# Performance work log

Measured on AMD Instinct MI355X. Metric: run time of the kernel, lower is better.

Reference implementation:

```python
import jax, jax.numpy as jnp
import numpy as np

EPS = 1e-5

def _ln(x, g, b):
    m = jnp.mean(x, axis=-1, keepdims=True)
    v = jnp.var(x, axis=-1, keepdims=True)
    return (x - m) / jnp.sqrt(v + EPS) * g + b

def _partition(x, nw):
    b, h, w, c = x.shape
    x = x.reshape(b, nw, h // nw, nw, w // nw, c).transpose(0, 1, 3, 2, 4, 5)
    return x.reshape(b * nw * nw, h // nw, w // nw, c)

def _merge(x, nw):
    b_, h, w, c = x.shape
    b = b_ // (nw * nw)
    x = x.reshape(b, nw, nw, h, w, c).transpose(0, 1, 3, 2, 4, 5)
    return x.reshape(b, nw * h, nw * w, c)

def _window_attn(q, k, v, width, height, nw, mask):
    b, _, c = q.shape
    q = q.reshape(b, height, width, c)
    k = k.reshape(b, height, width, c)
    v = v.reshape(b, height, width, c)
    sh, sw = (height // nw) // 2, (width // nw) // 2
    q = jnp.roll(q, (-sh, -sw), (1, 2))
    k = jnp.roll(k, (-sh, -sw), (1, 2))
    v = jnp.roll(v, (-sh, -sw), (1, 2))
    q = _partition(q, nw); k = _partition(k, nw); v = _partition(v, nw)
    N = (height // nw) * (width // nw)
    b_ = b * nw * nw
    qf = q.reshape(b_, N, c); kf = k.reshape(b_, N, c); vf = v.reshape(b_, N, c)
    scale = jnp.asarray(c, qf.dtype) ** 0.5
    scores = jnp.einsum('bnc,bmc->bnm', qf, kf) / scale  # [b_, N, N]
    scores = (scores.reshape(b, nw * nw, N, N) + mask[None]).reshape(b_, N, N)
    attn = jax.nn.softmax(scores, axis=-1)
    out = jnp.einsum('bnm,bmc->bnc', attn, vf)
    out = _merge(out.reshape(b_, height // nw, width // nw, c), nw)
    out = jnp.roll(out, (sh, sw), (1, 2))
    return out.reshape(b, height * width, c)

def _block(feat0, feat1, width, height, mask, nw, wq, wk, wv, wfc, g, be, ffn=None):
    q = feat0 @ wq; k = feat1 @ wk; v = feat1 @ wv
    a = _window_attn(q, k, v, width, height, nw, mask)
    a = _ln(a @ wfc, g, be)
    if ffn is not None:
        w1, w2, fg, fb = ffn
        h = jax.nn.gelu(jnp.concatenate([feat0, a], axis=-1) @ w1, approximate=False)
        a = _ln(h @ w2, fg, fb)
    return feat0 + a

def setup_inputs() -> dict:
    key = jax.random.key(0)
    B, H, W, NW, D = 8, 128, 128, 8, 256
    N = (H // NW) * (W // NW)
    ks = jax.random.split(key, 16)
    s = D ** -0.5
    return {
        'feat0': jax.random.normal(ks[0], (B, H * W, D), jnp.float32),
        'feat1': jax.random.normal(ks[1], (B, H * W, D), jnp.float32),
        'mask_attn': jax.random.normal(ks[2], (NW * NW, N, N), jnp.float32),
        'width': W, 'height': H, 'n_window': NW,
        'intra_wq': jax.random.normal(ks[3], (D, D), jnp.float32) * s,
        'intra_wk': jax.random.normal(ks[4], (D, D), jnp.float32) * s,
        'intra_wv': jax.random.normal(ks[5], (D, D), jnp.float32) * s,
        'intra_wfc': jax.random.normal(ks[6], (D, D), jnp.float32) * s,
        'intra_g': jnp.ones((D,), jnp.float32),
        'intra_b': jnp.zeros((D,), jnp.float32),
        'inter_wq': jax.random.normal(ks[7], (D, D), jnp.float32) * s,
        'inter_wk': jax.random.normal(ks[8], (D, D), jnp.float32) * s,
        'inter_wv': jax.random.normal(ks[9], (D, D), jnp.float32) * s,
        'inter_wfc': jax.random.normal(ks[10], (D, D), jnp.float32) * s,
        'inter_g': jnp.ones((D,), jnp.float32),
        'inter_b': jnp.zeros((D,), jnp.float32),
        'inter_w1': jax.random.normal(ks[11], (2 * D, 2 * D * 4), jnp.float32) * (2 * D) ** -0.5,
        'inter_w2': jax.random.normal(ks[12], (2 * D * 4, D), jnp.float32) * (2 * D * 4) ** -0.5,
        'inter_fg': jnp.ones((D,), jnp.float32),
        'inter_fb': jnp.zeros((D,), jnp.float32),
    }

def reference(feat0, feat1, mask_attn, width, height, n_window,
              intra_wq, intra_wk, intra_wv, intra_wfc, intra_g, intra_b,
              inter_wq, inter_wk, inter_wv, inter_wfc, inter_g, inter_b,
              inter_w1, inter_w2, inter_fg, inter_fb):
    f0 = _block(feat0, feat0, width, height, mask_attn, n_window,
                intra_wq, intra_wk, intra_wv, intra_wfc, intra_g, intra_b)
    out = _block(f0, feat1, width, height, mask_attn, n_window,
                 inter_wq, inter_wk, inter_wv, inter_wfc, inter_g, inter_b,
                 ffn=(inter_w1, inter_w2, inter_fg, inter_fb))
    return out
```

## Files before the change

### kernel.cpp

```cpp
#include <hip/hip_runtime.h>

typedef unsigned short u16;
typedef unsigned int   u32;

using f32x4  = __attribute__((ext_vector_type(4))) float;
using bf16x8 = __attribute__((ext_vector_type(8))) __bf16;

__device__ inline u16 f2bf(float f) {
  return __builtin_bit_cast(u16, (__bf16)f);
}
__device__ inline float bf2f(u16 v) {
  u32 u = ((u32)v) << 16;
  return __builtin_bit_cast(float, u);
}
__device__ inline u32 pk_bf16(float a, float b) {
  u32 d;
  asm("v_cvt_pk_bf16_f32 %0, %1, %2" : "=v"(d) : "v"(a), "v"(b));
  return d;
}

__device__ inline void gl_lds16(const u16* g, u16* l) {
  __builtin_amdgcn_global_load_lds((const __attribute__((address_space(1))) void*)g,
                                   (__attribute__((address_space(3))) void*)l,
                                   16, 0, 0);
}

__device__ inline int perm_fwd(int m) {
  int b = m >> 14, rem = m & 16383;
  int h = rem >> 7, w = rem & 127;
  int hr = (h - 8) & 127, wr = (w - 8) & 127;
  int win = (b << 6) | ((hr >> 4) << 3) | (wr >> 4);
  return (win << 8) | ((hr & 15) << 4) | (wr & 15);
}
__device__ inline int perm_inv(int r) {
  int win = r >> 8, t = r & 255;
  int b = win >> 6, wy = (win >> 3) & 7, wx = win & 7;
  int h = (((wy << 4) | (t >> 4)) + 8) & 127;
  int w = (((wx << 4) | (t & 15)) + 8) & 127;
  return (b << 14) | (h << 7) | w;
}


enum { MODE_QKV = 0, MODE_PV = 2, MODE_FFN1 = 4 };

template<int MODE>
__global__ __launch_bounds__(256)
void gemm_nt(const u16* __restrict__ A, int lda, long long sAz,
             const u16* __restrict__ Bt, int ldb, long long sBz,
             u16* __restrict__ OutB, float* __restrict__ OutF,
             const float* __restrict__ mask, int K, int ldo)
{
  __shared__ __align__(16) u16 sA[128 * 64];
  __shared__ __align__(16) u16 sB[128 * 64];

  const int tid  = threadIdx.x;
  const int lane = tid & 63;
  const int wave = tid >> 6;
  const int l15  = lane & 15;
  const int quad = lane >> 4;
  const int wm   = (wave >> 1) << 6;
  const int wn   = (wave & 1) << 6;
  const int z    = blockIdx.z;
  const int m0   = (int)(blockIdx.y) << 7;
  const int n0   = (int)(blockIdx.x) << 7;

  const u16* Ab = A  + (long long)z * sAz;
  const u16* Bb = Bt + (long long)z * sBz;

  const int cd = ((lane & 7) ^ ((lane >> 3) & 7)) << 3;
  const int rs = (wave << 5) + (lane >> 3);
  const u16* ga0 = Ab + (long long)(m0 + rs) * lda + cd;
  const u16* gb0 = Bb + (long long)(n0 + rs) * ldb + cd;
  u16* la0 = &sA[wave << 11];
  u16* lb0 = &sB[wave << 11];

  const f32x4 zero = {0.f, 0.f, 0.f, 0.f};
  f32x4 acc[4][4];
#pragma unroll
  for (int i = 0; i < 4; ++i)
#pragma unroll
    for (int j = 0; j < 4; ++j) acc[i][j] = zero;

  for (int k0 = 0; k0 < K; k0 += 64) {
    __syncthreads();
#pragma unroll
    for (int p = 0; p < 4; ++p) {
      gl_lds16(ga0 + k0 + (p << 3) * lda, la0 + (p << 9));
      gl_lds16(gb0 + k0 + (p << 3) * ldb, lb0 + (p << 9));
    }
    __syncthreads();
#pragma unroll
    for (int kk = 0; kk < 2; ++kk) {
      const int sw = (((quad | (kk << 2)) ^ (l15 & 7)) << 3);
      bf16x8 af[4], bfr[4];
#pragma unroll
      for (int i = 0; i < 4; ++i) {
        af[i]  = *(const bf16x8*)(sA + ((wm + (i << 4) + l15) << 6) + sw);
        bfr[i] = *(const bf16x8*)(sB + ((wn + (i << 4) + l15) << 6) + sw);
      }
#pragma unroll
      for (int i = 0; i < 4; ++i)
#pragma unroll
        for (int j = 0; j < 4; ++j)
          acc[i][j] = __builtin_amdgcn_mfma_f32_16x16x32_bf16(af[i], bfr[j], acc[i][j], 0, 0, 0);
    }
  }

#pragma unroll
  for (int i = 0; i < 4; ++i) {
#pragma unroll
    for (int r = 0; r < 4; ++r) {
      int mg = m0 + wm + (i << 4) + (quad << 2) + r;
      if constexpr (MODE == MODE_QKV) {
        u16* orow = OutB + (long long)(n0 >> 8) * ldo + ((long long)perm_fwd(mg) << 8);
        uint2 d;
        d.x = pk_bf16(acc[i][0][r], acc[i][1][r]);
        d.y = pk_bf16(acc[i][2][r], acc[i][3][r]);
        *(uint2*)(orow + (n0 & 128) + wn + (l15 << 2)) = d;
      } else if constexpr (MODE == MODE_PV) {
        u16* orow = OutB + ((long long)perm_inv((z << 8) + mg) << 8);
        uint2 d;
        d.x = pk_bf16(acc[i][0][r], acc[i][1][r]);
        d.y = pk_bf16(acc[i][2][r], acc[i][3][r]);
        *(uint2*)(orow + n0 + wn + (l15 << 2)) = d;
      } else {
        float gv[4];
#pragma unroll
        for (int j = 0; j < 4; ++j) {
          float v = acc[i][j][r];
          float t = v * fmaf(v * v, -0.071354816f, -1.5957691216f);
          gv[j] = v * __builtin_amdgcn_rcpf(1.0f + __expf(t));
        }
        uint2 d;
        d.x = pk_bf16(gv[0], gv[1]);
        d.y = pk_bf16(gv[2], gv[3]);
        *(uint2*)(OutB + (long long)mg * ldo + n0 + wn + (l15 << 2)) = d;
      }
    }
  }
}

__global__ __launch_bounds__(256)
void gemm_vt(const u16* __restrict__ Wt,
             const u16* __restrict__ Feat,
             u16* __restrict__ Vt)
{
  __shared__ __align__(16) u16 sA[128 * 64];
  __shared__ __align__(16) u16 sB[128 * 64];

  const int tid  = threadIdx.x;
  const int lane = tid & 63;
  const int wave = tid >> 6;
  const int l15  = lane & 15;
  const int quad = lane >> 4;
  const int wm   = (wave >> 1) << 6;
  const int wn   = (wave & 1) << 6;
  const int z    = blockIdx.z;
  const int m0   = (int)(blockIdx.y) << 7;
  const int n0   = (int)(blockIdx.x) << 7;

  const int cd = ((lane & 7) ^ ((lane >> 3) & 7)) << 3;
  const int rs = (wave << 5) + (lane >> 3);
  const u16* ga0 = Wt + (long long)(m0 + rs) * 256 + cd;
  const u16* gb0 = Feat + (long long)perm_inv((z << 8) + n0 + rs)        * 256 + cd;
  const u16* gb1 = Feat + (long long)perm_inv((z << 8) + n0 + rs + 8)    * 256 + cd;
  const u16* gb2 = Feat + (long long)perm_inv((z << 8) + n0 + rs + 16)   * 256 + cd;
  const u16* gb3 = Feat + (long long)perm_inv((z << 8) + n0 + rs + 24)   * 256 + cd;
  u16* la0 = &sA[wave << 11];
  u16* lb0 = &sB[wave << 11];

  const f32x4 zero = {0.f, 0.f, 0.f, 0.f};
  f32x4 acc[4][4];
#pragma unroll
  for (int i = 0; i < 4; ++i)
#pragma unroll
    for (int j = 0; j < 4; ++j) acc[i][j] = zero;

  for (int k0 = 0; k0 < 256; k0 += 64) {
    __syncthreads();
#pragma unroll
    for (int p = 0; p < 4; ++p)
      gl_lds16(ga0 + k0 + (p << 3) * 256, la0 + (p << 9));
    gl_lds16(gb0 + k0, lb0);
    gl_lds16(gb1 + k0, lb0 + 512);
    gl_lds16(gb2 + k0, lb0 + 1024);
    gl_lds16(gb3 + k0, lb0 + 1536);
    __syncthreads();
#pragma unroll
    for (int kk = 0; kk < 2; ++kk) {
      const int sw = (((quad | (kk << 2)) ^ (l15 & 7)) << 3);
      bf16x8 af[4], bfr[4];
#pragma unroll
      for (int i = 0; i < 4; ++i) {
        af[i]  = *(const bf16x8*)(sA + ((wm + (i << 4) + l15) << 6) + sw);
        bfr[i] = *(const bf16x8*)(sB + ((wn + (i << 4) + l15) << 6) + sw);
      }
#pragma unroll
      for (int i = 0; i < 4; ++i)
#pragma unroll
        for (int j = 0; j < 4; ++j)
          acc[i][j] = __builtin_amdgcn_mfma_f32_16x16x32_bf16(af[i], bfr[j], acc[i][j], 0, 0, 0);
    }
  }

#pragma unroll
  for (int i = 0; i < 4; ++i) {
#pragma unroll
    for (int r = 0; r < 4; ++r) {
      const int mg = m0 + wm + (i << 4) + (quad << 2) + r;
      u16* orow = Vt + (((long long)z) << 16) + ((long long)mg << 8);
#pragma unroll
      for (int j = 0; j < 4; ++j) {
        int ng = n0 + wn + (j << 4) + l15;
        orow[ng] = f2bf(acc[i][j][r]);
      }
    }
  }
}

__global__ __launch_bounds__(256)
void scores_softmax(const u16* __restrict__ Q, const u16* __restrict__ Kw,
                    const float* __restrict__ mask, u16* __restrict__ SP)
{
  __shared__ __align__(16) u16 sA[128 * 64];
  __shared__ __align__(16) u16 sB[256 * 64];

  const int tid  = threadIdx.x;
  const int lane = tid & 63;
  const int wave = tid >> 6;
  const int l15  = lane & 15;
  const int quad = lane >> 4;

  const int mhalf = (int)blockIdx.x;
  const int z     = (int)blockIdx.y;
  const int m0    = mhalf << 7;

  const u16* Ab = Q  + ((long long)z << 16);
  const u16* Bb = Kw + ((long long)z << 16);

  const int cd  = ((lane & 7) ^ ((lane >> 3) & 7)) << 3;
  const int rsA = (wave << 5) + (lane >> 3);
  const int rsB = (wave << 6) + (lane >> 3);
  const u16* ga0 = Ab + (long long)(m0 + rsA) * 256 + cd;
  const u16* gb0 = Bb + (long long)rsB * 256 + cd;
  u16* la0 = &sA[wave << 11];
  u16* lb0 = &sB[wave << 12];

  const f32x4 zero = {0.f, 0.f, 0.f, 0.f};
  f32x4 acc[2][16];
#pragma unroll
  for (int i = 0; i < 2; ++i)
#pragma unroll
    for (int j = 0; j < 16; ++j) acc[i][j] = zero;

  for (int k0 = 0; k0 < 256; k0 += 64) {
    __syncthreads();
#pragma unroll
    for (int p = 0; p < 4; ++p)
      gl_lds16(ga0 + k0 + (p << 3) * 256, la0 + (p << 9));
#pragma unroll
    for (int p = 0; p < 8; ++p)
      gl_lds16(gb0 + k0 + (p << 3) * 256, lb0 + (p << 9));
    __syncthreads();
#pragma unroll
    for (int kk = 0; kk < 2; ++kk) {
      const int sw = (((quad | (kk << 2)) ^ (l15 & 7)) << 3);
      bf16x8 af0 = *(const bf16x8*)(sA + (((wave << 5) + l15) << 6) + sw);
      bf16x8 af1 = *(const bf16x8*)(sA + (((wave << 5) + 16 + l15) << 6) + sw);
#pragma unroll
      for (int j = 0; j < 16; ++j) {
        bf16x8 bf = *(const bf16x8*)(sB + (((j << 4) + l15) << 6) + sw);
        acc[0][j] = __builtin_amdgcn_mfma_f32_16x16x32_bf16(af0, bf, acc[0][j], 0, 0, 0);
        acc[1][j] = __builtin_amdgcn_mfma_f32_16x16x32_bf16(af1, bf, acc[1][j], 0, 0, 0);
      }
    }
  }

  const float* mbase = mask + (((long long)(z & 63)) << 16);
#pragma unroll
  for (int i = 0; i < 2; ++i) {
#pragma unroll
    for (int r = 0; r < 4; ++r) {
      const int mg = m0 + (wave << 5) + (i << 4) + (quad << 2) + r;
      const float* mrow = mbase + ((long long)mg << 8);
      float sv[16];
      float mx = -3.0e38f;
#pragma unroll
      for (int j = 0; j < 16; ++j) {
        sv[j] = acc[i][j][r] * 0.0625f + mrow[(j << 4) + l15];
        mx = fmaxf(mx, sv[j]);
      }
#pragma unroll
      for (int o = 1; o < 16; o <<= 1) mx = fmaxf(mx, __shfl_xor(mx, o));
      float sum = 0.f;
#pragma unroll
      for (int j = 0; j < 16; ++j) { sv[j] = __expf(sv[j] - mx); sum += sv[j]; }
#pragma unroll
      for (int o = 1; o < 16; o <<= 1) sum += __shfl_xor(sum, o);
      const float inv = 1.0f / sum;
      u16* orow = SP + (((long long)z) << 16) + ((long long)mg << 8);
#pragma unroll
      for (int j = 0; j < 16; ++j) orow[(j << 4) + l15] = f2bf(sv[j] * inv);
    }
  }
}

enum { LN_XCAT0 = 0, LN_XCAT1 = 1, LN_OUT = 2 };

template<int MODE>
__global__ __launch_bounds__(256)
void gemm_ln(const u16* __restrict__ A, int lda,
             const u16* __restrict__ Bt,
             const float* __restrict__ G, const float* __restrict__ Bias,
             const float* __restrict__ ResF, const u16* __restrict__ ResB,
             float* __restrict__ OutF, u16* __restrict__ OutB, int K)
{
  __shared__ __align__(16) u16 sA[64 * 64];
  __shared__ __align__(16) u16 sB[256 * 64];

  const int tid  = threadIdx.x;
  const int lane = tid & 63;
  const int wave = tid >> 6;
  const int l15  = lane & 15;
  const int quad = lane >> 4;
  const int m0   = (int)blockIdx.x << 6;

  const int cd  = ((lane & 7) ^ ((lane >> 3) & 7)) << 3;
  const int rsA = (wave << 4) + (lane >> 3);
  const int rsB = (wave << 6) + (lane >> 3);
  const u16* ga0 = A  + (long long)(m0 + rsA) * lda + cd;
  const u16* gb0 = Bt + (long long)rsB * K + cd;
  u16* la0 = &sA[wave << 10];
  u16* lb0 = &sB[wave << 12];

  const f32x4 zero = {0.f, 0.f, 0.f, 0.f};
  f32x4 acc[16];
#pragma unroll
  for (int j = 0; j < 16; ++j) acc[j] = zero;

  for (int k0 = 0; k0 < K; k0 += 64) {
    __syncthreads();
#pragma unroll
    for (int p = 0; p < 2; ++p)
      gl_lds16(ga0 + k0 + (p << 3) * lda, la0 + (p << 9));
#pragma unroll
    for (int p = 0; p < 8; ++p)
      gl_lds16(gb0 + k0 + (p << 3) * K, lb0 + (p << 9));
    __syncthreads();
#pragma unroll
    for (int kk = 0; kk < 2; ++kk) {
      const int sw = (((quad | (kk << 2)) ^ (l15 & 7)) << 3);
      bf16x8 af = *(const bf16x8*)(sA + (((wave << 4) + l15) << 6) + sw);
#pragma unroll
      for (int j = 0; j < 16; ++j) {
        bf16x8 bf = *(const bf16x8*)(sB + (((j << 4) + l15) << 6) + sw);
        acc[j] = __builtin_amdgcn_mfma_f32_16x16x32_bf16(af, bf, acc[j], 0, 0, 0);
      }
    }
  }

  float gj[16], bj[16];
#pragma unroll
  for (int j = 0; j < 16; ++j) {
    gj[j] = G[(j << 4) + l15];
    bj[j] = Bias[(j << 4) + l15];
  }

#pragma unroll
  for (int r = 0; r < 4; ++r) {
    const int mg = m0 + (wave << 4) + (quad << 2) + r;
    float s = 0.f, s2 = 0.f;
#pragma unroll
    for (int j = 0; j < 16; ++j) {
      float v = acc[j][r];
      s += v; s2 += v * v;
    }
#pragma unroll
    for (int o = 1; o < 16; o <<= 1) { s += __shfl_xor(s, o); s2 += __shfl_xor(s2, o); }
    const float mean = s * (1.0f / 256.0f);
    const float var  = s2 * (1.0f / 256.0f) - mean * mean;
    const float rstd = rsqrtf(var + 1e-5f);
    if constexpr (MODE == LN_XCAT0) {
      u16* orow = OutB + ((long long)mg << 9);
      const float* rrow = ResF + ((long long)mg << 8);
#pragma unroll
      for (int j = 0; j < 16; ++j) {
        float v = (acc[j][r] - mean) * rstd * gj[j] + bj[j];
        orow[(j << 4) + l15] = f2bf(v + rrow[(j << 4) + l15]);
      }
    } else if constexpr (MODE == LN_XCAT1) {
      u16* orow = OutB + ((long long)mg << 9) + 256;
#pragma unroll
      for (int j = 0; j < 16; ++j) {
        float v = (acc[j][r] - mean) * rstd * gj[j] + bj[j];
        orow[(j << 4) + l15] = f2bf(v);
      }
    } else {
      const u16* rrow = ResB + ((long long)mg << 9);
      float* orow = OutF + ((long long)mg << 8);
#pragma unroll
      for (int j = 0; j < 16; ++j) {
        float v = (acc[j][r] - mean) * rstd * gj[j] + bj[j];
        orow[(j << 4) + l15] = v + bf2f(rrow[(j << 4) + l15]);
      }
    }
  }
}

__global__ __launch_bounds__(256)
void cvt_f32_bf16(const float* __restrict__ src, u16* __restrict__ dst, int n4)
{
  int i = blockIdx.x * 256 + threadIdx.x;
  if (i >= n4) return;
  float4 v = ((const float4*)src)[i];
  ushort4 u; u.x = f2bf(v.x); u.y = f2bf(v.y); u.z = f2bf(v.z); u.w = f2bf(v.w);
  ((ushort4*)dst)[i] = u;
}

__global__ __launch_bounds__(256)
void wtrans(const float* __restrict__ src, u16* __restrict__ dst, int R, int C)
{
  int idx = blockIdx.x * 256 + threadIdx.x;
  if (idx >= R * C) return;
  int r = idx / C, c = idx - r * C;
  dst[c * R + r] = f2bf(src[idx]);
}

__global__ __launch_bounds__(256)
void wtrans_sig(const float* __restrict__ src, u16* __restrict__ dst)
{
  int idx = blockIdx.x * 256 + threadIdx.x;
  int n = idx >> 8, q = idx & 255;
  int f = (q & ~63) | ((q & 3) << 4) | ((q >> 2) & 15);
  dst[idx] = f2bf(src[f * 256 + n]);
}

__global__ __launch_bounds__(256)
void wtrans_w2(const float* __restrict__ src, u16* __restrict__ dst)
{
  int idx = blockIdx.x * 256 + threadIdx.x;
  int c = idx >> 11, q = idx & 2047;
  int f = (q & ~63) | ((q & 3) << 4) | ((q >> 2) & 15);
  dst[idx] = f2bf(src[f * 256 + c]);
}

extern "C" void kernel_launch(void* const* d_in, const int* in_sizes, int n_in,
                              void* d_out, int out_size, void* d_ws, size_t ws_size,
                              hipStream_t stream)
{
  (void)in_sizes; (void)n_in; (void)out_size;
  const float* feat0 = (const float*)d_in[0];
  const float* feat1 = (const float*)d_in[1];
  const float* mask  = (const float*)d_in[2];
  const float* wq1 = (const float*)d_in[6];
  const float* wk1 = (const float*)d_in[7];
  const float* wv1 = (const float*)d_in[8];
  const float* wf1 = (const float*)d_in[9];
  const float* g1  = (const float*)d_in[10];
  const float* b1  = (const float*)d_in[11];
  const float* wq2 = (const float*)d_in[12];
  const float* wk2 = (const float*)d_in[13];
  const float* wv2 = (const float*)d_in[14];
  const float* wf2 = (const float*)d_in[15];
  const float* g2  = (const float*)d_in[16];
  const float* b2  = (const float*)d_in[17];
  const float* w1  = (const float*)d_in[18];
  const float* w2  = (const float*)d_in[19];
  const float* fg  = (const float*)d_in[20];
  const float* fb  = (const float*)d_in[21];

  const size_t Mi = 1048576;
  const size_t WB = 4 * Mi;
  const int Mtot = 131072;

  int nc = 8;
  for (int c = 1; c <= 8; c <<= 1) {
    size_t S = (size_t)(Mtot / c) * 512;
    if (7 * S + WB <= ws_size) { nc = c; break; }
  }
  const int Mc = Mtot / nc;
  const size_t S = (size_t)Mc * 512;

  char* ws = (char*)d_ws;
  u16*   featb = (u16*)(ws);
  u16*   SPb   = featb;
  u16*   qw    = (u16*)(ws + S);
  u16*   Ob    = qw;
  u16*   hbuf  = featb;
  u16*   kw    = (u16*)(ws + 2 * S);
  u16*   vt    = (u16*)(ws + 4 * S);
  u16*   xcat  = (u16*)(ws + 5 * S);
  u16*   wb    = (u16*)(ws + 7 * S);
  u16* wq1t = wb;            u16* wk1t = wb + 65536;  u16* wv1t = wb + 131072; u16* wf1t = wb + 196608;
  u16* wq2t = wb + 262144;   u16* wk2t = wb + 327680; u16* wv2t = wb + 393216; u16* wf2t = wb + 458752;
  u16* w1t  = wb + 524288;
  u16* w2t  = wb + 524288 + 1048576;

  const dim3 blk(256);
  const dim3 gBig(2, Mc / 128, 1);
  const dim3 gQK(4, Mc / 128, 1);
  const int  Wc = Mc / 256;
  const dim3 gWin(2, 2, Wc);
  const dim3 gSS(2, Wc);
  const int  gRows = Mc / 4;
  const int  gLN   = Mc / 64;
  const int  MF = Mc / 2;
  const dim3 gF1(16, MF / 128, 1);
  const int  gLNF  = MF / 64;

  wtrans<<<256, blk, 0, stream>>>(wq1, wq1t, 256, 256);
  wtrans<<<256, blk, 0, stream>>>(wk1, wk1t, 256, 256);
  wtrans<<<256, blk, 0, stream>>>(wv1, wv1t, 256, 256);
  wtrans_sig<<<256, blk, 0, stream>>>(wf1, wf1t);
  wtrans<<<256, blk, 0, stream>>>(wq2, wq2t, 256, 256);
  wtrans<<<256, blk, 0, stream>>>(wk2, wk2t, 256, 256);
  wtrans<<<256, blk, 0, stream>>>(wv2, wv2t, 256, 256);
  wtrans_sig<<<256, blk, 0, stream>>>(wf2, wf2t);
  wtrans<<<4096, blk, 0, stream>>>(w1, w1t, 512, 2048);
  wtrans_w2<<<2048, blk, 0, stream>>>(w2, w2t);

  const int qkStride = Mc * 256;

  for (int c = 0; c < nc; ++c) {
    const long long off = (long long)c * Mc * 256;
    const float* f0in = feat0 + off;
    const float* f1in = feat1 + off;
    float* outp = (float*)d_out + off;

    cvt_f32_bf16<<<gRows, blk, 0, stream>>>(f0in, featb, Mc * 64);
    gemm_nt<MODE_QKV><<<gQK, blk, 0, stream>>>(featb, 256, 0, wq1t, 256, 0, qw, nullptr, nullptr, 256, qkStride);
    gemm_vt<<<gWin, blk, 0, stream>>>(wv1t, featb, vt);
    scores_softmax<<<gSS, blk, 0, stream>>>(qw, kw, mask, SPb);
    gemm_nt<MODE_PV><<<gWin, blk, 0, stream>>>(SPb, 256, 65536, vt, 256, 65536, Ob, nullptr, nullptr, 256, 0);
    gemm_ln<LN_XCAT0><<<gLN, blk, 0, stream>>>(Ob, 256, wf1t, g1, b1, f0in, nullptr, nullptr, xcat, 256);

    cvt_f32_bf16<<<gRows, blk, 0, stream>>>(f1in, featb, Mc * 64);
    gemm_nt<MODE_QKV><<<gBig, blk, 0, stream>>>(xcat, 512, 0, wq2t, 256, 0, qw, nullptr, nullptr, 512, 0);
    gemm_nt<MODE_QKV><<<gBig, blk, 0, stream>>>(featb, 256, 0, wk2t, 256, 0, kw, nullptr, nullptr, 256, 0);
    gemm_vt<<<gWin, blk, 0, stream>>>(wv2t, featb, vt);
    scores_softmax<<<gSS, blk, 0, stream>>>(qw, kw, mask, SPb);
    gemm_nt<MODE_PV><<<gWin, blk, 0, stream>>>(SPb, 256, 65536, vt, 256, 65536, Ob, nullptr, nullptr, 256, 0);
    gemm_ln<LN_XCAT1><<<gLN, blk, 0, stream>>>(Ob, 256, wf2t, g2, b2, nullptr, nullptr, nullptr, xcat, 256);

    for (int mc = 0; mc < 2; ++mc) {
      const u16* xc = xcat + (long long)mc * MF * 512;
      gemm_nt<MODE_FFN1><<<gF1, blk, 0, stream>>>(xc, 512, 0, w1t, 512, 0,
                                                  hbuf, nullptr, nullptr, 512, 2048);
      gemm_ln<LN_OUT><<<gLNF, blk, 0, stream>>>(hbuf, 2048, w2t, fg, fb, nullptr,
                                                xcat + (long long)mc * MF * 512,
                                                outp + (long long)mc * MF * 256, nullptr, 2048);
    }
  }
}
```

Measured before the change: 1.632 ms.

## Triple-buffer GEMM K-loop with 32-wide stages and async LDS prefetch

Replaces the synchronous two-barrier K-loop in gemm_nt and gemm_vt with a three-slot LDS ring of 32-wide K stages. Global-to-LDS loads for later stages are issued before computing the current one, with vmcnt waits and a single barrier per stage. It also changes the LDS layout and XOR swizzle to fit 32-column tiles. The aim is to hide global load latency behind MFMA work, at the cost of more LDS per block, which may reduce occupancy.

```diff
diff --git a/kernel.cpp b/kernel.cpp
--- a/kernel.cpp
+++ b/kernel.cpp
@@ -50,8 +50,8 @@
              u16* __restrict__ OutB, float* __restrict__ OutF,
              const float* __restrict__ mask, int K, int ldo)
 {
-  __shared__ __align__(16) u16 sA[128 * 64];
-  __shared__ __align__(16) u16 sB[128 * 64];
+  __shared__ __align__(16) u16 sA[3 * 4096];
+  __shared__ __align__(16) u16 sB[3 * 4096];
 
   const int tid  = threadIdx.x;
   const int lane = tid & 63;
@@ -67,12 +67,17 @@
   const u16* Ab = A  + (long long)z * sAz;
   const u16* Bb = Bt + (long long)z * sBz;
 
-  const int cd = ((lane & 7) ^ ((lane >> 3) & 7)) << 3;
-  const int rs = (wave << 5) + (lane >> 3);
-  const u16* ga0 = Ab + (long long)(m0 + rs) * lda + cd;
-  const u16* gb0 = Bb + (long long)(n0 + rs) * ldb + cd;
-  u16* la0 = &sA[wave << 11];
-  u16* lb0 = &sB[wave << 11];
+  const int r_in = ((lane >> 3) << 1) | ((lane >> 2) & 1);
+  const int cdE  = ((lane & 3) ^ ((lane >> 3) & 3)) << 3;
+  const u16* gaq0 = Ab + (long long)(m0 + (wave << 5) + r_in) * lda + cdE;
+  const u16* gaq1 = gaq0 + 16ll * lda;
+  const u16* gbq0 = Bb + (long long)(n0 + (wave << 5) + r_in) * ldb + cdE;
+  const u16* gbq1 = gbq0 + 16ll * ldb;
+  const int dst0 = wave << 10;
+  const int dst1 = dst0 + 512;
+
+  const int slotlo = quad ^ ((l15 >> 1) & 3);
+  const int fr = ((l15 >> 1) << 6) + ((((l15 & 1) << 2) | slotlo) << 3);
 
   const f32x4 zero = {0.f, 0.f, 0.f, 0.f};
   f32x4 acc[4][4];
@@ -81,30 +86,50 @@
 #pragma unroll
     for (int j = 0; j < 4; ++j) acc[i][j] = zero;
 
-  for (int k0 = 0; k0 < K; k0 += 64) {
-    __syncthreads();
-#pragma unroll
-    for (int p = 0; p < 4; ++p) {
-      gl_lds16(ga0 + k0 + (p << 3) * lda, la0 + (p << 9));
-      gl_lds16(gb0 + k0 + (p << 3) * ldb, lb0 + (p << 9));
-    }
-    __syncthreads();
-#pragma unroll
-    for (int kk = 0; kk < 2; ++kk) {
-      const int sw = (((quad | (kk << 2)) ^ (l15 & 7)) << 3);
-      bf16x8 af[4], bfr[4];
-#pragma unroll
-      for (int i = 0; i < 4; ++i) {
-        af[i]  = *(const bf16x8*)(sA + ((wm + (i << 4) + l15) << 6) + sw);
-        bfr[i] = *(const bf16x8*)(sB + ((wn + (i << 4) + l15) << 6) + sw);
-      }
-#pragma unroll
-      for (int i = 0; i < 4; ++i)
-#pragma unroll
-        for (int j = 0; j < 4; ++j)
-          acc[i][j] = __builtin_amdgcn_mfma_f32_16x16x32_bf16(af[i], bfr[j], acc[i][j], 0, 0, 0);
-    }
-  }
+  auto STAGE = [&](int slot, int col) {
+    const int b = slot << 12;
+    gl_lds16(gaq0 + col, &sA[b + dst0]);
+    gl_lds16(gaq1 + col, &sA[b + dst1]);
+    gl_lds16(gbq0 + col, &sB[b + dst0]);
+    gl_lds16(gbq1 + col, &sB[b + dst1]);
+  };
+  auto COMPUTE = [&](int slot) {
+    const int b = slot << 12;
+    bf16x8 af[4], bfr[4];
+#pragma unroll
+    for (int i = 0; i < 4; ++i) {
+      af[i]  = *(const bf16x8*)(&sA[b + (wm << 5) + (i << 9) + fr]);
+      bfr[i] = *(const bf16x8*)(&sB[b + (wn << 5) + (i << 9) + fr]);
+    }
+#pragma unroll
+    for (int i = 0; i < 4; ++i)
+#pragma unroll
+      for (int j = 0; j < 4; ++j)
+        acc[i][j] = __builtin_amdgcn_mfma_f32_16x16x32_bf16(af[i], bfr[j], acc[i][j], 0, 0, 0);
+  };
+
+  STAGE(0, 0);
+  STAGE(1, 32);
+  asm volatile("s_waitcnt vmcnt(4)" ::: "memory");
+  __builtin_amdgcn_s_barrier();
+
+  int r0 = 0, r1 = 1;
+  for (int k0 = 0; k0 + 64 < K; k0 += 64) {
+    const int w0 = 3 - r0 - r1;
+    STAGE(w0, k0 + 64);
+    COMPUTE(r0);
+    asm volatile("s_waitcnt vmcnt(4)" ::: "memory");
+    __builtin_amdgcn_s_barrier();
+    STAGE(r0, k0 + 96);
+    COMPUTE(r1);
+    asm volatile("s_waitcnt vmcnt(4)" ::: "memory");
+    __builtin_amdgcn_s_barrier();
+    r1 = r0; r0 = w0;
+  }
+  COMPUTE(r0);
+  asm volatile("s_waitcnt vmcnt(0)" ::: "memory");
+  __builtin_amdgcn_s_barrier();
+  COMPUTE(r1);
 
 #pragma unroll
   for (int i = 0; i < 4; ++i) {
@@ -145,8 +170,8 @@
              const u16* __restrict__ Feat,
              u16* __restrict__ Vt)
 {
-  __shared__ __align__(16) u16 sA[128 * 64];
-  __shared__ __align__(16) u16 sB[128 * 64];
+  __shared__ __align__(16) u16 sA[3 * 4096];
+  __shared__ __align__(16) u16 sB[3 * 4096];
 
   const int tid  = threadIdx.x;
   const int lane = tid & 63;
@@ -159,15 +184,17 @@
   const int m0   = (int)(blockIdx.y) << 7;
   const int n0   = (int)(blockIdx.x) << 7;
 
-  const int cd = ((lane & 7) ^ ((lane >> 3) & 7)) << 3;
-  const int rs = (wave << 5) + (lane >> 3);
-  const u16* ga0 = Wt + (long long)(m0 + rs) * 256 + cd;
-  const u16* gb0 = Feat + (long long)perm_inv((z << 8) + n0 + rs)        * 256 + cd;
-  const u16* gb1 = Feat + (long long)perm_inv((z << 8) + n0 + rs + 8)    * 256 + cd;
-  const u16* gb2 = Feat + (long long)perm_inv((z << 8) + n0 + rs + 16)   * 256 + cd;
-  const u16* gb3 = Feat + (long long)perm_inv((z << 8) + n0 + rs + 24)   * 256 + cd;
-  u16* la0 = &sA[wave << 11];
-  u16* lb0 = &sB[wave << 11];
+  const int r_in = ((lane >> 3) << 1) | ((lane >> 2) & 1);
+  const int cdE  = ((lane & 3) ^ ((lane >> 3) & 3)) << 3;
+  const u16* gaq0 = Wt + (long long)(m0 + (wave << 5) + r_in) * 256 + cdE;
+  const u16* gaq1 = gaq0 + 16ll * 256;
+  const u16* gbq0 = Feat + (long long)perm_inv((z << 8) + n0 + (wave << 5) + r_in)      * 256 + cdE;
+  const u16* gbq1 = Feat + (long long)perm_inv((z << 8) + n0 + (wave << 5) + 16 + r_in) * 256 + cdE;
+  const int dst0 = wave << 10;
+  const int dst1 = dst0 + 512;
+
+  const int slotlo = quad ^ ((l15 >> 1) & 3);
+  const int fr = ((l15 >> 1) << 6) + ((((l15 & 1) << 2) | slotlo) << 3);
 
   const f32x4 zero = {0.f, 0.f, 0.f, 0.f};
   f32x4 acc[4][4];
@@ -176,32 +203,50 @@
 #pragma unroll
     for (int j = 0; j < 4; ++j) acc[i][j] = zero;
 
-  for (int k0 = 0; k0 < 256; k0 += 64) {
-    __syncthreads();
-#pragma unroll
-    for (int p = 0; p < 4; ++p)
-      gl_lds16(ga0 + k0 + (p << 3) * 256, la0 + (p << 9));
-    gl_lds16(gb0 + k0, lb0);
-    gl_lds16(gb1 + k0, lb0 + 512);
-    gl_lds16(gb2 + k0, lb0 + 1024);
-    gl_lds16(gb3 + k0, lb0 + 1536);
-    __syncthreads();
-#pragma unroll
-    for (int kk = 0; kk < 2; ++kk) {
-      const int sw = (((quad | (kk << 2)) ^ (l15 & 7)) << 3);
-      bf16x8 af[4], bfr[4];
-#pragma unroll
-      for (int i = 0; i < 4; ++i) {
-        af[i]  = *(const bf16x8*)(sA + ((wm + (i << 4) + l15) << 6) + sw);
-        bfr[i] = *(const bf16x8*)(sB + ((wn + (i << 4) + l15) << 6) + sw);
-      }
-#pragma unroll
-      for (int i = 0; i < 4; ++i)
-#pragma unroll
-        for (int j = 0; j < 4; ++j)
-          acc[i][j] = __builtin_amdgcn_mfma_f32_16x16x32_bf16(af[i], bfr[j], acc[i][j], 0, 0, 0);
-    }
-  }
+  auto STAGE = [&](int slot, int col) {
+    const int b = slot << 12;
+    gl_lds16(gaq0 + col, &sA[b + dst0]);
+    gl_lds16(gaq1 + col, &sA[b + dst1]);
+    gl_lds16(gbq0 + col, &sB[b + dst0]);
+    gl_lds16(gbq1 + col, &sB[b + dst1]);
+  };
+  auto COMPUTE = [&](int slot) {
+    const int b = slot << 12;
+    bf16x8 af[4], bfr[4];
+#pragma unroll
+    for (int i = 0; i < 4; ++i) {
+      af[i]  = *(const bf16x8*)(&sA[b + (wm << 5) + (i << 9) + fr]);
+      bfr[i] = *(const bf16x8*)(&sB[b + (wn << 5) + (i << 9) + fr]);
+    }
+#pragma unroll
+    for (int i = 0; i < 4; ++i)
+#pragma unroll
+      for (int j = 0; j < 4; ++j)
+        acc[i][j] = __builtin_amdgcn_mfma_f32_16x16x32_bf16(af[i], bfr[j], acc[i][j], 0, 0, 0);
+  };
+
+  STAGE(0, 0);
+  STAGE(1, 32);
+  asm volatile("s_waitcnt vmcnt(4)" ::: "memory");
+  __builtin_amdgcn_s_barrier();
+
+  int r0 = 0, r1 = 1;
+  for (int k0 = 0; k0 + 64 < 256; k0 += 64) {
+    const int w0 = 3 - r0 - r1;
+    STAGE(w0, k0 + 64);
+    COMPUTE(r0);
+    asm volatile("s_waitcnt vmcnt(4)" ::: "memory");
+    __builtin_amdgcn_s_barrier();
+    STAGE(r0, k0 + 96);
+    COMPUTE(r1);
+    asm volatile("s_waitcnt vmcnt(4)" ::: "memory");
+    __builtin_amdgcn_s_barrier();
+    r1 = r0; r0 = w0;
+  }
+  COMPUTE(r0);
+  asm volatile("s_waitcnt vmcnt(0)" ::: "memory");
+  __builtin_amdgcn_s_barrier();
+  COMPUTE(r1);
 
 #pragma unroll
   for (int i = 0; i < 4; ++i) {
```

Measured after the change: 1.699 ms. 4.1% more time.

## Add dedicated 256x256-tile 8-wave pipelined GEMM kernel for FFN1 with fused GELU

Applied to the files above, without the earlier changes.

Replaces the generic 128-tile gemm_nt FFN1 path with a specialised kernel that uses 512 threads (8 waves) and a 256x256 output tile. K=512 is split into 32-wide half-phases, with double-buffered global-to-LDS loads interleaved between MFMA phases and explicit vmcnt waits and barriers. It also uses s_setprio around the MFMA bursts. The goal is more operand reuse per LDS load and better overlap of memory with compute on the largest GEMM. In exchange it brings heavy register pressure (128 accumulator floats per thread), fewer blocks in the grid, and hand-tuned wait counts that are fragile.

```diff
diff --git a/kernel.cpp b/kernel.cpp
--- a/kernel.cpp
+++ b/kernel.cpp
@@ -136,6 +136,128 @@
         d.y = pk_bf16(gv[2], gv[3]);
         *(uint2*)(OutB + (long long)mg * ldo + n0 + wn + (l15 << 2)) = d;
       }
+    }
+  }
+}
+
+
+#define STA8(buf, kh, k) { gl_lds16(gA0 + (k), &sA[buf][kh][dq0]); \
+                           gl_lds16(gA1 + (k), &sA[buf][kh][dq1]); }
+#define STB8(buf, kh, k) { gl_lds16(gB0 + (k), &sB[buf][kh][dq0]); \
+                           gl_lds16(gB1 + (k), &sB[buf][kh][dq1]); }
+#define PHASE8(buf, kk, qn) { \
+    bf16x8 af[8], bfq[2]; \
+    _Pragma("unroll") \
+    for (int i = 0; i < 8; ++i) \
+      af[i] = *(const bf16x8*)(&sA[buf][kk][((wmw + (i << 4) + l15) << 5) + fr]); \
+    _Pragma("unroll") \
+    for (int jc = 0; jc < 2; ++jc) \
+      bfq[jc] = *(const bf16x8*)(&sB[buf][kk][((wnw + ((qn) << 5) + (jc << 4) + l15) << 5) + fr]); \
+    __builtin_amdgcn_s_setprio(1); \
+    _Pragma("unroll") \
+    for (int i = 0; i < 8; ++i) { \
+      acc[i][((qn) << 1) | 0] = __builtin_amdgcn_mfma_f32_16x16x32_bf16(af[i], bfq[0], acc[i][((qn) << 1) | 0], 0, 0, 0); \
+      acc[i][((qn) << 1) | 1] = __builtin_amdgcn_mfma_f32_16x16x32_bf16(af[i], bfq[1], acc[i][((qn) << 1) | 1], 0, 0, 0); \
+    } \
+    __builtin_amdgcn_s_setprio(0); }
+
+__global__ __launch_bounds__(512, 2)
+void gemm_ffn1_8p(const u16* __restrict__ A, int lda,
+                  const u16* __restrict__ Bt, int ldb,
+                  u16* __restrict__ OutB, int ldo)
+{
+  __shared__ __align__(16) u16 sA[2][2][8192];
+  __shared__ __align__(16) u16 sB[2][2][8192];
+
+  const int tid  = threadIdx.x;
+  const int lane = tid & 63;
+  const int wave = tid >> 6;
+  const int l15  = lane & 15;
+  const int quad = lane >> 4;
+  const int wmw  = (wave >> 2) << 7;
+  const int wnw  = (wave & 3) << 6;
+  const int m0   = (int)blockIdx.y << 8;
+  const int n0   = (int)blockIdx.x << 8;
+
+  const int cd  = ((lane & 3) ^ ((lane >> 3) & 3)) << 3;
+  const int rq0 = (wave << 5) + (lane >> 2);
+  const u16* gA0 = A  + (long long)(m0 + rq0) * lda + cd;
+  const u16* gA1 = gA0 + 16ll * lda;
+  const u16* gB0 = Bt + (long long)(n0 + rq0) * ldb + cd;
+  const u16* gB1 = gB0 + 16ll * ldb;
+  const int dq0 = wave << 10;
+  const int dq1 = dq0 + 512;
+
+  const int fr = ((quad ^ ((l15 >> 1) & 3)) << 3);
+
+  const f32x4 zero = {0.f, 0.f, 0.f, 0.f};
+  f32x4 acc[8][4];
+#pragma unroll
+  for (int i = 0; i < 8; ++i)
+#pragma unroll
+    for (int j = 0; j < 4; ++j) acc[i][j] = zero;
+
+  STA8(0, 0, 0);  STB8(0, 0, 0);
+  STA8(0, 1, 32); STB8(0, 1, 32);
+  STA8(1, 0, 64); STB8(1, 0, 64);
+  asm volatile("s_waitcnt vmcnt(8)" ::: "memory");
+  __builtin_amdgcn_s_barrier();
+
+  for (int T = 0; T < 6; ++T) {
+    const int buf = T & 1, nb = buf ^ 1;
+    const int kb = T << 6;
+    STA8(nb, 1, kb + 96);
+    PHASE8(buf, 0, 0);
+    __builtin_amdgcn_s_barrier();
+    STB8(nb, 1, kb + 96);
+    PHASE8(buf, 0, 1);
+    asm volatile("s_waitcnt vmcnt(8)" ::: "memory");
+    __builtin_amdgcn_s_barrier();
+    STA8(buf, 0, kb + 128);
+    PHASE8(buf, 1, 0);
+    __builtin_amdgcn_s_barrier();
+    STB8(buf, 0, kb + 128);
+    PHASE8(buf, 1, 1);
+    asm volatile("s_waitcnt vmcnt(8)" ::: "memory");
+    __builtin_amdgcn_s_barrier();
+  }
+  STA8(1, 1, 480);
+  PHASE8(0, 0, 0);
+  __builtin_amdgcn_s_barrier();
+  STB8(1, 1, 480);
+  PHASE8(0, 0, 1);
+  asm volatile("s_waitcnt vmcnt(8)" ::: "memory");
+  __builtin_amdgcn_s_barrier();
+  PHASE8(0, 1, 0);
+  __builtin_amdgcn_s_barrier();
+  PHASE8(0, 1, 1);
+  asm volatile("s_waitcnt vmcnt(4)" ::: "memory");
+  __builtin_amdgcn_s_barrier();
+  PHASE8(1, 0, 0);
+  __builtin_amdgcn_s_barrier();
+  PHASE8(1, 0, 1);
+  asm volatile("s_waitcnt vmcnt(0)" ::: "memory");
+  __builtin_amdgcn_s_barrier();
+  PHASE8(1, 1, 0);
+  __builtin_amdgcn_s_barrier();
+  PHASE8(1, 1, 1);
+
+#pragma unroll
+  for (int i = 0; i < 8; ++i) {
+#pragma unroll
+    for (int r = 0; r < 4; ++r) {
+      const int mg = m0 + wmw + (i << 4) + (quad << 2) + r;
+      float gv[4];
+#pragma unroll
+      for (int j = 0; j < 4; ++j) {
+        float v = acc[i][j][r];
+        float t = v * fmaf(v * v, -0.071354816f, -1.5957691216f);
+        gv[j] = v * __builtin_amdgcn_rcpf(1.0f + __expf(t));
+      }
+      uint2 d;
+      d.x = pk_bf16(gv[0], gv[1]);
+      d.y = pk_bf16(gv[2], gv[3]);
+      *(uint2*)(OutB + (long long)mg * ldo + n0 + wnw + (l15 << 2)) = d;
     }
   }
 }
@@ -505,7 +627,8 @@
   const int  gRows = Mc / 4;
   const int  gLN   = Mc / 64;
   const int  MF = Mc / 2;
-  const dim3 gF1(16, MF / 128, 1);
+  const dim3 gF1(8, MF / 256, 1);
+  const dim3 blk512(512);
   const int  gLNF  = MF / 64;
 
   wtrans<<<256, blk, 0, stream>>>(wq1, wq1t, 256, 256);
@@ -544,8 +667,7 @@
 
     for (int mc = 0; mc < 2; ++mc) {
       const u16* xc = xcat + (long long)mc * MF * 512;
-      gemm_nt<MODE_FFN1><<<gF1, blk, 0, stream>>>(xc, 512, 0, w1t, 512, 0,
-                                                  hbuf, nullptr, nullptr, 512, 2048);
+      gemm_ffn1_8p<<<gF1, blk512, 0, stream>>>(xc, 512, w1t, 512, hbuf, 2048);
       gemm_ln<LN_OUT><<<gLNF, blk, 0, stream>>>(hbuf, 2048, w2t, fg, fb, nullptr,
                                                 xcat + (long long)mc * MF * 512,
                                                 outp + (long long)mc * MF * 256, nullptr, 2048);
```

Result: slower. 1.684 ms (+3.2%).
